# Kernel optimization log

Hardware: AMD Instinct MI355X
Metric: run time of the kernel (lower is better)

## Reference

```python
import jax, jax.numpy as jnp
import numpy as np

# ---- static config (matches torch module defaults) ----
SPATIAL = np.array([[100, 100], [50, 50], [25, 25], [13, 13]], dtype=np.int64)  # [L,2] (H,W)
EMBED, HEADS, LEVELS, POINTS = 256, 8, 4, 4
HEAD_DIM = EMBED // HEADS
TOTAL_POINTS = HEADS * LEVELS * POINTS
BS, LQ = 32, 300
LV = int((SPATIAL[:, 0] * SPATIAL[:, 1]).sum())  # 13294


def setup_inputs() -> dict:
    key = jax.random.key(0)
    ks = jax.random.split(key, 12)
    s = 1.0 / np.sqrt(EMBED)
    return {
        "query": jax.random.normal(ks[0], (BS, LQ, EMBED), jnp.float32),
        "reference_points": jax.random.uniform(ks[1], (BS, LQ, LEVELS, 2), jnp.float32),
        "value": jax.random.normal(ks[2], (BS, LV, EMBED), jnp.float32),
        "value_spatial_shapes": jnp.asarray(SPATIAL),
        # learned parameters (torch: Linear weight [out,in] -> stored here as [in,out])
        "W_off": jax.random.normal(ks[3], (EMBED, TOTAL_POINTS * 2), jnp.float32) * 0.01,
        "b_off": jax.random.normal(ks[4], (TOTAL_POINTS * 2,), jnp.float32) * 0.01,
        "W_attn": jax.random.normal(ks[5], (EMBED, TOTAL_POINTS), jnp.float32) * s,
        "b_attn": jnp.zeros((TOTAL_POINTS,), jnp.float32),
        "W_val": jax.random.normal(ks[6], (EMBED, EMBED), jnp.float32) * s,
        "b_val": jnp.zeros((EMBED,), jnp.float32),
        "W_out": jax.random.normal(ks[7], (EMBED, EMBED), jnp.float32) * s,
        "b_out": jnp.zeros((EMBED,), jnp.float32),
    }


def _bilinear_sample(v, grid, H, W):
    """F.grid_sample(mode='bilinear', padding_mode='zeros', align_corners=False).
    v: [H*W, c], grid: [Lq, P, 2] in [-1, 1] (x, y). Returns [Lq, P, c]."""
    x = (grid[..., 0] + 1.0) * 0.5 * W - 0.5
    y = (grid[..., 1] + 1.0) * 0.5 * H - 0.5
    x0f, y0f = jnp.floor(x), jnp.floor(y)
    lx, ly = x - x0f, y - y0f
    x0, y0 = x0f.astype(jnp.int32), y0f.astype(jnp.int32)

    def gather(iy, ix):
        valid = ((iy >= 0) & (iy < H) & (ix >= 0) & (ix < W)).astype(v.dtype)[..., None]
        idx = jnp.clip(iy, 0, H - 1) * W + jnp.clip(ix, 0, W - 1)
        return v[idx] * valid

    return (gather(y0, x0) * ((1 - ly) * (1 - lx))[..., None]
            + gather(y0, x0 + 1) * ((1 - ly) * lx)[..., None]
            + gather(y0 + 1, x0) * (ly * (1 - lx))[..., None]
            + gather(y0 + 1, x0 + 1) * (ly * lx)[..., None])


def _ms_deform_attn_core(value, sampling_grids, attention_weights):
    """value: [bs, Lv, H, c]; sampling_grids: [bs, Lq, H, L, P, 2] in [-1,1];
    attention_weights: [bs, Lq, H, L, P] -> output [bs, Lq, H*c]."""
    bs, Lq = sampling_grids.shape[:2]
    samples = []
    start = 0
    for lvl in range(LEVELS):
        H, W = int(SPATIAL[lvl, 0]), int(SPATIAL[lvl, 1])
        # [bs, HW, nh, c] -> [bs*nh, HW, c]
        v_l = value[:, start:start + H * W]
        v_l = v_l.transpose(0, 2, 1, 3).reshape(bs * HEADS, H * W, HEAD_DIM)
        # [bs, Lq, nh, P, 2] -> [bs*nh, Lq, P, 2]
        g_l = sampling_grids[:, :, :, lvl].transpose(0, 2, 1, 3, 4).reshape(bs * HEADS, Lq, POINTS, 2)
        samples.append(jax.vmap(lambda vv, gg: _bilinear_sample(vv, gg, H, W))(v_l, g_l))
        start += H * W
    stacked = jnp.stack(samples, axis=2)  # [bs*nh, Lq, L, P, c]
    aw = attention_weights.transpose(0, 2, 1, 3, 4).reshape(bs * HEADS, Lq, LEVELS, POINTS)
    out = (stacked * aw[..., None]).sum(axis=(2, 3))  # [bs*nh, Lq, c]
    return out.reshape(bs, HEADS, Lq, HEAD_DIM).transpose(0, 2, 1, 3).reshape(bs, Lq, EMBED)


def reference(query, reference_points, value, value_spatial_shapes,
              W_off, b_off, W_attn, b_attn, W_val, b_val, W_out, b_out):
    bs, Lq = query.shape[:2]
    Lv = value.shape[1]

    value_p = (value @ W_val + b_val).reshape(bs, Lv, HEADS, HEAD_DIM)

    offsets = (query @ W_off + b_off).reshape(bs, Lq, HEADS, LEVELS, POINTS, 2)
    attn = jax.nn.softmax((query @ W_attn + b_attn).reshape(bs, Lq, HEADS, LEVELS * POINTS), axis=-1)
    attn = attn.reshape(bs, Lq, HEADS, LEVELS, POINTS)

    # offset_normalizer = flip(spatial_shapes) -> (W, H) per level
    norm = jnp.asarray(SPATIAL[:, ::-1].copy(), jnp.float32)  # [L, 2]
    sampling_locations = (reference_points[:, :, None, :, None, :]
                          + offsets / norm[None, None, None, :, None, :])
    sampling_grids = 2.0 * sampling_locations - 1.0

    out = _ms_deform_attn_core(value_p, sampling_grids, attn)
    return out @ W_out + b_out
```

## Files before the change

kernel.cpp:

```cpp
#include <hip/hip_runtime.h>
#include <hip/hip_bf16.h>

#define BS_   32
#define LQ_   300
#define LV_   13294
#define EMBED_ 256
#define HEADS_ 8
#define HEAD_DIM_ 32
#define NCHUNK_ 13294
#define PSTRIDE_ 512

typedef __attribute__((ext_vector_type(8))) short bf16x8;
typedef __attribute__((ext_vector_type(4))) float f32x4;

__device__ inline short f2bf(float f) {
  union { float f; unsigned u; } x; x.f = f;
  return (short)((x.u + 0x7FFF + ((x.u >> 16) & 1)) >> 16);
}
__device__ inline short f2bf_i(float f) {
  union { __hip_bfloat16 h; short s; } u;
  u.h = __float2bfloat16(f);
  return u.s;
}
__device__ inline float bf2f(short s) {
  union { unsigned u; float f; } x; x.u = ((unsigned)(unsigned short)s) << 16;
  return x.f;
}

__device__ __forceinline__ void gld_lds16(const void* g, void* l) {
  __builtin_amdgcn_global_load_lds(
      (const __attribute__((address_space(1))) unsigned int*)g,
      (__attribute__((address_space(3))) unsigned int*)l, 16, 0, 0);
}

__global__ void convert_wt(const float* __restrict__ W, short* __restrict__ Wt,
                           int Nsrc) {
  const int n = blockIdx.x;
  const int k = threadIdx.x;
  Wt[n * 256 + k] = (n < Nsrc) ? f2bf(W[k * Nsrc + n]) : (short)0;
}

__global__ __launch_bounds__(512, 2) void gemm_value_persist(
    const float* __restrict__ A, const short* __restrict__ Wt,
    const float* __restrict__ bias, short* __restrict__ Vp) {
  __shared__ float As[2][32 * 256];

  const int tid = threadIdx.x;
  const int lane = tid & 63;
  const int w = tid >> 6;
  const int lr = lane & 15;
  const int lkq = lane >> 4;

  bf16x8 bfr[2][8];
#pragma unroll
  for (int nf = 0; nf < 2; ++nf) {
    const size_t bbase = (size_t)(w * 32 + nf * 16 + lr) * 256 + lkq * 8;
#pragma unroll
    for (int kt = 0; kt < 8; ++kt)
      bfr[nf][kt] = *(const bf16x8*)(Wt + bbase + kt * 32);
  }
  float bv[2];
#pragma unroll
  for (int nf = 0; nf < 2; ++nf) bv[nf] = bias[w * 32 + nf * 16 + lr];

  auto stage = [&](int buf, int c) {
    const float* src = A + (size_t)c * (32 * 256);
#pragma unroll
    for (int i = 0; i < 4; ++i) {
      const int r = w * 4 + i;
      gld_lds16(src + r * 256 + ((lane ^ (r & 7)) * 4), &As[buf][r * 256]);
    }
  };

  const int c0 = blockIdx.x;
  stage(0, c0);
  asm volatile("s_waitcnt vmcnt(0)" ::: "memory");
  __syncthreads();

  int cb = 0;
  for (int c = c0; c < NCHUNK_; c += PSTRIDE_) {
    const int nxt = c + PSTRIDE_;
    if (nxt < NCHUNK_) stage(cb ^ 1, nxt);

    f32x4 acc[2][2];
#pragma unroll
    for (int i = 0; i < 2; ++i)
#pragma unroll
      for (int jj = 0; jj < 2; ++jj) acc[i][jj] = (f32x4){0.f, 0.f, 0.f, 0.f};

    const float* as = &As[cb][0];
#pragma unroll
    for (int kt = 0; kt < 8; ++kt) {
      const int r0 = lr;
      const int r1 = 16 + lr;
      const int g = kt * 8 + lkq * 2;
      const f32x4 a00 = *(const f32x4*)(as + r0 * 256 + (((g    ) ^ (r0 & 7)) * 4));
      const f32x4 a01 = *(const f32x4*)(as + r0 * 256 + (((g + 1) ^ (r0 & 7)) * 4));
      const f32x4 a10 = *(const f32x4*)(as + r1 * 256 + (((g    ) ^ (r1 & 7)) * 4));
      const f32x4 a11 = *(const f32x4*)(as + r1 * 256 + (((g + 1) ^ (r1 & 7)) * 4));
      bf16x8 af0, af1;
#pragma unroll
      for (int i = 0; i < 4; ++i) {
        af0[i]     = f2bf_i(a00[i]);
        af0[i + 4] = f2bf_i(a01[i]);
        af1[i]     = f2bf_i(a10[i]);
        af1[i + 4] = f2bf_i(a11[i]);
      }
      acc[0][0] = __builtin_amdgcn_mfma_f32_16x16x32_bf16(af0, bfr[0][kt], acc[0][0], 0, 0, 0);
      acc[0][1] = __builtin_amdgcn_mfma_f32_16x16x32_bf16(af0, bfr[1][kt], acc[0][1], 0, 0, 0);
      acc[1][0] = __builtin_amdgcn_mfma_f32_16x16x32_bf16(af1, bfr[0][kt], acc[1][0], 0, 0, 0);
      acc[1][1] = __builtin_amdgcn_mfma_f32_16x16x32_bf16(af1, bfr[1][kt], acc[1][1], 0, 0, 0);
    }

#pragma unroll
    for (int mf = 0; mf < 2; ++mf)
#pragma unroll
      for (int rr = 0; rr < 4; ++rr) {
        const unsigned m = (unsigned)c * 32 + mf * 16 + lkq * 4 + rr;
        const unsigned b_ = m / LV_;
        const unsigned pos = m - b_ * LV_;
        const size_t rowbase = ((size_t)(b_ * HEADS_ + w) * LV_ + pos) * HEAD_DIM_;
#pragma unroll
        for (int nf = 0; nf < 2; ++nf)
          Vp[rowbase + nf * 16 + lr] = f2bf(acc[mf][nf][rr] + bv[nf]);
      }

    if (nxt < NCHUNK_) {
      asm volatile("s_waitcnt vmcnt(16)" ::: "memory");
      asm volatile("s_barrier" ::: "memory");
    }
    cb ^= 1;
  }
}

__global__ __launch_bounds__(256, 2) void gemm_qproj(
    const float* __restrict__ A, const short* __restrict__ Wt,
    const float* __restrict__ bias, float* __restrict__ C,
    int ldc, int Nbias) {
  __shared__ float As[64 * 256];

  const int tid = threadIdx.x;
  const int lane = tid & 63;
  const int w = tid >> 6;
  const int n0 = w * 64;
  const size_t m0 = (size_t)blockIdx.x * 64;
  const int lr = lane & 15;
  const int lkq = lane >> 4;

#pragma unroll
  for (int i = 0; i < 16; ++i) {
    const int row = w * 16 + i;
    gld_lds16(A + (m0 + row) * 256 + ((lane ^ (row & 7)) * 4), As + row * 256);
  }

  bf16x8 bfr[4][8];
#pragma unroll
  for (int nf = 0; nf < 4; ++nf) {
    const size_t bbase = (size_t)(n0 + nf * 16 + lr) * 256 + lkq * 8;
#pragma unroll
    for (int kt = 0; kt < 8; ++kt)
      bfr[nf][kt] = *(const bf16x8*)(Wt + bbase + kt * 32);
  }

  f32x4 acc[4][4];
#pragma unroll
  for (int i = 0; i < 4; ++i)
#pragma unroll
    for (int jj = 0; jj < 4; ++jj) acc[i][jj] = (f32x4){0.f, 0.f, 0.f, 0.f};

  __syncthreads();

#pragma unroll
  for (int kt = 0; kt < 8; ++kt) {
#pragma unroll
    for (int mf = 0; mf < 4; ++mf) {
      const int row = mf * 16 + lr;
      const int gbase = kt * 8 + lkq * 2;
      const f32x4 a0 = *(const f32x4*)(As + row * 256 + ((gbase) ^ (row & 7)) * 4);
      const f32x4 a1 = *(const f32x4*)(As + row * 256 + ((gbase + 1) ^ (row & 7)) * 4);
      bf16x8 af;
#pragma unroll
      for (int i = 0; i < 4; ++i) {
        af[i]     = f2bf_i(a0[i]);
        af[i + 4] = f2bf_i(a1[i]);
      }
#pragma unroll
      for (int nf = 0; nf < 4; ++nf)
        acc[mf][nf] = __builtin_amdgcn_mfma_f32_16x16x32_bf16(af, bfr[nf][kt], acc[mf][nf], 0, 0, 0);
    }
  }

  float bv[4];
#pragma unroll
  for (int nf = 0; nf < 4; ++nf) {
    const int n = n0 + nf * 16 + lr;
    bv[nf] = (n < Nbias) ? bias[n] : 0.f;
  }
  const int lq4 = lkq * 4;
#pragma unroll
  for (int mf = 0; mf < 4; ++mf)
#pragma unroll
    for (int r = 0; r < 4; ++r) {
      const size_t m = m0 + mf * 16 + lq4 + r;
#pragma unroll
      for (int nf = 0; nf < 4; ++nf) {
        const int n = n0 + nf * 16 + lr;
        C[m * ldc + n] = acc[mf][nf][r] + bv[nf];
      }
    }
}

__global__ void softmax16(const float* __restrict__ logits,
                          float* __restrict__ attn, int ngroups) {
  const int g = blockIdx.x * blockDim.x + threadIdx.x;
  if (g >= ngroups) return;
  const int row = g >> 3, h = g & 7;
  const float* in = logits + (size_t)row * 256 + h * 16;
  float v[16];
  float m = -1e30f;
#pragma unroll
  for (int i = 0; i < 16; ++i) { v[i] = in[i]; m = fmaxf(m, v[i]); }
  float s = 0.f;
#pragma unroll
  for (int i = 0; i < 16; ++i) { v[i] = __expf(v[i] - m); s += v[i]; }
  const float inv = 1.0f / s;
  float* out = attn + (size_t)g * 16;
#pragma unroll
  for (int i = 0; i < 16; ++i) out[i] = v[i] * inv;
}

__global__ __launch_bounds__(256) void msda_sample(
    const float* __restrict__ ref_pts,
    const float* __restrict__ offsets,
    const float* __restrict__ attn,
    const short* __restrict__ value_p,
    float* __restrict__ tmp)
{
  const int t = blockIdx.x * 256 + threadIdx.x;
  const int c8 = t & 3;
  const int h = (t >> 2) & 7;
  const int row = t >> 5;
  const int b = row / LQ_;

  const int HS[4] = {100, 50, 25, 13};
  const int START[4] = {0, 10000, 12500, 13125};

  const float* offr = offsets + (size_t)row * 256 + h * 32;
  const float* attr = attn + (size_t)row * 128 + h * 16;
  const float* refr = ref_pts + (size_t)row * 8;

  float acc[8];
#pragma unroll
  for (int jj = 0; jj < 8; ++jj) acc[jj] = 0.f;

#pragma unroll
  for (int l = 0; l < 4; ++l) {
    const int HH = HS[l];
    const int WW = HS[l];
    const float fH = (float)HH, fW = (float)WW;
    const float rx = refr[l * 2 + 0];
    const float ry = refr[l * 2 + 1];
    const short* vbase =
        value_p + ((size_t)(b * HEADS_ + h) * LV_ + START[l]) * HEAD_DIM_ + c8 * 8;
#pragma unroll
    for (int p = 0; p < 4; ++p) {
      const float ox = offr[(l * 4 + p) * 2 + 0];
      const float oy = offr[(l * 4 + p) * 2 + 1];
      const float x = (rx + ox / fW) * fW - 0.5f;
      const float y = (ry + oy / fH) * fH - 0.5f;
      const float x0f = floorf(x), y0f = floorf(y);
      const float fx = x - x0f, fy = y - y0f;
      const int x0 = (int)x0f, y0 = (int)y0f;
      const float wgt = attr[l * 4 + p];
      const float iy0 = (y0 >= 0 && y0 < HH) ? 1.f : 0.f;
      const float iy1 = (y0 + 1 >= 0 && y0 + 1 < HH) ? 1.f : 0.f;
      const float ix0 = (x0 >= 0 && x0 < WW) ? 1.f : 0.f;
      const float ix1 = (x0 + 1 >= 0 && x0 + 1 < WW) ? 1.f : 0.f;
      const float w00 = (1.f - fy) * (1.f - fx) * wgt * iy0 * ix0;
      const float w01 = (1.f - fy) * fx * wgt * iy0 * ix1;
      const float w10 = fy * (1.f - fx) * wgt * iy1 * ix0;
      const float w11 = fy * fx * wgt * iy1 * ix1;
      const int xc0 = min(max(x0, 0), WW - 1);
      const int xc1 = min(max(x0 + 1, 0), WW - 1);
      const int yc0 = min(max(y0, 0), HH - 1);
      const int yc1 = min(max(y0 + 1, 0), HH - 1);
      const bf16x8 q00 = *(const bf16x8*)(vbase + (size_t)(yc0 * WW + xc0) * HEAD_DIM_);
      const bf16x8 q01 = *(const bf16x8*)(vbase + (size_t)(yc0 * WW + xc1) * HEAD_DIM_);
      const bf16x8 q10 = *(const bf16x8*)(vbase + (size_t)(yc1 * WW + xc0) * HEAD_DIM_);
      const bf16x8 q11 = *(const bf16x8*)(vbase + (size_t)(yc1 * WW + xc1) * HEAD_DIM_);
#pragma unroll
      for (int jj = 0; jj < 8; ++jj) {
        acc[jj] += w00 * bf2f(q00[jj]) + w01 * bf2f(q01[jj]) +
                   w10 * bf2f(q10[jj]) + w11 * bf2f(q11[jj]);
      }
    }
  }
  float* o = tmp + (size_t)row * 256 + h * 32 + c8 * 8;
  f32x4 o0 = {acc[0], acc[1], acc[2], acc[3]};
  f32x4 o1 = {acc[4], acc[5], acc[6], acc[7]};
  *(f32x4*)(o) = o0;
  *(f32x4*)(o + 4) = o1;
}

extern "C" void kernel_launch(void* const* d_in, const int* in_sizes, int n_in,
                              void* d_out, int out_size, void* d_ws, size_t ws_size,
                              hipStream_t stream) {
  const float* query  = (const float*)d_in[0];
  const float* refpts = (const float*)d_in[1];
  const float* value  = (const float*)d_in[2];
  const float* W_off  = (const float*)d_in[4];
  const float* b_off  = (const float*)d_in[5];
  const float* W_attn = (const float*)d_in[6];
  const float* b_attn = (const float*)d_in[7];
  const float* W_val  = (const float*)d_in[8];
  const float* b_val  = (const float*)d_in[9];
  const float* W_out  = (const float*)d_in[10];
  const float* b_out  = (const float*)d_in[11];
  float* out = (float*)d_out;

  char* ws = (char*)d_ws;
  short* value_p = (short*)ws;
  size_t off = (size_t)BS_ * HEADS_ * LV_ * HEAD_DIM_ * 2;
  float* offsets = (float*)(ws + off); off += (size_t)BS_ * LQ_ * 256 * 4;
  float* attn    = (float*)(ws + off); off += (size_t)BS_ * LQ_ * 128 * 4;
  float* tmp     = (float*)(ws + off); off += (size_t)BS_ * LQ_ * 256 * 4;

  short* WtA = (short*)value_p;
  short* WtB = (short*)value_p + 256 * 256;
  float* logits = tmp;
  short* WtV = (short*)tmp;
  short* WtO = (short*)value_p;

  const int MQ = BS_ * LQ_;

  convert_wt<<<256, 256, 0, stream>>>(W_off, WtA, 256);
  convert_wt<<<256, 256, 0, stream>>>(W_attn, WtB, 128);
  gemm_qproj<<<MQ / 64, 256, 0, stream>>>(query, WtA, b_off, offsets, 256, 256);
  gemm_qproj<<<MQ / 64, 256, 0, stream>>>(query, WtB, b_attn, logits, 256, 128);
  softmax16<<<(MQ * HEADS_ + 255) / 256, 256, 0, stream>>>(logits, attn, MQ * HEADS_);
  convert_wt<<<256, 256, 0, stream>>>(W_val, WtV, 256);
  gemm_value_persist<<<PSTRIDE_, 512, 0, stream>>>(value, WtV, b_val, value_p);
  msda_sample<<<(MQ * 32) / 256, 256, 0, stream>>>(refpts, offsets, attn, value_p, tmp);
  convert_wt<<<256, 256, 0, stream>>>(W_out, WtO, 256);
  gemm_qproj<<<MQ / 64, 256, 0, stream>>>(tmp, WtO, b_out, out, 256, 256);
}
```

Baseline: 228.1 us.

## Fuse offset/attn projections into one GEMM and fold softmax into sampler

```diff
diff --git a/kernel.cpp b/kernel.cpp
--- a/kernel.cpp
+++ b/kernel.cpp
@@ -38,6 +38,15 @@
   const int n = blockIdx.x;
   const int k = threadIdx.x;
   Wt[n * 256 + k] = (n < Nsrc) ? f2bf(W[k * Nsrc + n]) : (short)0;
+}
+
+__global__ void convert_wq(const float* __restrict__ W_off,
+                           const float* __restrict__ W_attn,
+                           short* __restrict__ Wt) {
+  const int n = blockIdx.x;
+  const int k = threadIdx.x;
+  Wt[n * 256 + k] = (n < 256) ? f2bf(W_off[k * 256 + n])
+                              : f2bf(W_attn[k * 128 + (n - 256)]);
 }
 
 __global__ __launch_bounds__(512, 2) void gemm_value_persist(
@@ -133,10 +142,10 @@
   }
 }
 
-__global__ __launch_bounds__(256, 2) void gemm_qproj(
+__global__ __launch_bounds__(384, 2) void gemm_qproj2(
     const float* __restrict__ A, const short* __restrict__ Wt,
-    const float* __restrict__ bias, float* __restrict__ C,
-    int ldc, int Nbias) {
+    const float* __restrict__ b_off, const float* __restrict__ b_attn,
+    float* __restrict__ offs, float* __restrict__ logits) {
   __shared__ float As[64 * 256];
 
   const int tid = threadIdx.x;
@@ -147,10 +156,12 @@
   const int lr = lane & 15;
   const int lkq = lane >> 4;
 
-#pragma unroll
-  for (int i = 0; i < 16; ++i) {
-    const int row = w * 16 + i;
-    gld_lds16(A + (m0 + row) * 256 + ((lane ^ (row & 7)) * 4), As + row * 256);
+  if (w < 4) {
+#pragma unroll
+    for (int i = 0; i < 16; ++i) {
+      const int row = w * 16 + i;
+      gld_lds16(A + (m0 + row) * 256 + ((lane ^ (row & 7)) * 4), As + row * 256);
+    }
   }
 
   bf16x8 bfr[4][8];
@@ -194,7 +205,7 @@
 #pragma unroll
   for (int nf = 0; nf < 4; ++nf) {
     const int n = n0 + nf * 16 + lr;
-    bv[nf] = (n < Nbias) ? bias[n] : 0.f;
+    bv[nf] = (n < 256) ? b_off[n] : b_attn[n - 256];
   }
   const int lq4 = lkq * 4;
 #pragma unroll
@@ -205,53 +216,123 @@
 #pragma unroll
       for (int nf = 0; nf < 4; ++nf) {
         const int n = n0 + nf * 16 + lr;
-        C[m * ldc + n] = acc[mf][nf][r] + bv[nf];
-      }
-    }
-}
-
-__global__ void softmax16(const float* __restrict__ logits,
-                          float* __restrict__ attn, int ngroups) {
-  const int g = blockIdx.x * blockDim.x + threadIdx.x;
-  if (g >= ngroups) return;
-  const int row = g >> 3, h = g & 7;
-  const float* in = logits + (size_t)row * 256 + h * 16;
-  float v[16];
-  float m = -1e30f;
-#pragma unroll
-  for (int i = 0; i < 16; ++i) { v[i] = in[i]; m = fmaxf(m, v[i]); }
-  float s = 0.f;
-#pragma unroll
-  for (int i = 0; i < 16; ++i) { v[i] = __expf(v[i] - m); s += v[i]; }
-  const float inv = 1.0f / s;
-  float* out = attn + (size_t)g * 16;
-#pragma unroll
-  for (int i = 0; i < 16; ++i) out[i] = v[i] * inv;
-}
-
-__global__ __launch_bounds__(256) void msda_sample(
+        if (n < 256) offs[m * 256 + n] = acc[mf][nf][r] + bv[nf];
+        else         logits[m * 128 + (n - 256)] = acc[mf][nf][r] + bv[nf];
+      }
+    }
+}
+
+__global__ __launch_bounds__(256, 2) void gemm_qproj(
+    const float* __restrict__ A, const short* __restrict__ Wt,
+    const float* __restrict__ bias, float* __restrict__ C) {
+  __shared__ float As[64 * 256];
+
+  const int tid = threadIdx.x;
+  const int lane = tid & 63;
+  const int w = tid >> 6;
+  const int n0 = w * 64;
+  const size_t m0 = (size_t)blockIdx.x * 64;
+  const int lr = lane & 15;
+  const int lkq = lane >> 4;
+
+#pragma unroll
+  for (int i = 0; i < 16; ++i) {
+    const int row = w * 16 + i;
+    gld_lds16(A + (m0 + row) * 256 + ((lane ^ (row & 7)) * 4), As + row * 256);
+  }
+
+  bf16x8 bfr[4][8];
+#pragma unroll
+  for (int nf = 0; nf < 4; ++nf) {
+    const size_t bbase = (size_t)(n0 + nf * 16 + lr) * 256 + lkq * 8;
+#pragma unroll
+    for (int kt = 0; kt < 8; ++kt)
+      bfr[nf][kt] = *(const bf16x8*)(Wt + bbase + kt * 32);
+  }
+
+  f32x4 acc[4][4];
+#pragma unroll
+  for (int i = 0; i < 4; ++i)
+#pragma unroll
+    for (int jj = 0; jj < 4; ++jj) acc[i][jj] = (f32x4){0.f, 0.f, 0.f, 0.f};
+
+  __syncthreads();
+
+#pragma unroll
+  for (int kt = 0; kt < 8; ++kt) {
+#pragma unroll
+    for (int mf = 0; mf < 4; ++mf) {
+      const int row = mf * 16 + lr;
+      const int gbase = kt * 8 + lkq * 2;
+      const f32x4 a0 = *(const f32x4*)(As + row * 256 + ((gbase) ^ (row & 7)) * 4);
+      const f32x4 a1 = *(const f32x4*)(As + row * 256 + ((gbase + 1) ^ (row & 7)) * 4);
+      bf16x8 af;
+#pragma unroll
+      for (int i = 0; i < 4; ++i) {
+        af[i]     = f2bf_i(a0[i]);
+        af[i + 4] = f2bf_i(a1[i]);
+      }
+#pragma unroll
+      for (int nf = 0; nf < 4; ++nf)
+        acc[mf][nf] = __builtin_amdgcn_mfma_f32_16x16x32_bf16(af, bfr[nf][kt], acc[mf][nf], 0, 0, 0);
+    }
+  }
+
+  float bv[4];
+#pragma unroll
+  for (int nf = 0; nf < 4; ++nf) bv[nf] = bias[n0 + nf * 16 + lr];
+  const int lq4 = lkq * 4;
+#pragma unroll
+  for (int mf = 0; mf < 4; ++mf)
+#pragma unroll
+    for (int r = 0; r < 4; ++r) {
+      const size_t m = m0 + mf * 16 + lq4 + r;
+#pragma unroll
+      for (int nf = 0; nf < 4; ++nf) {
+        const int n = n0 + nf * 16 + lr;
+        C[m * 256 + n] = acc[mf][nf][r] + bv[nf];
+      }
+    }
+}
+
+__global__ __launch_bounds__(256) void msda_sample_fused(
     const float* __restrict__ ref_pts,
     const float* __restrict__ offsets,
-    const float* __restrict__ attn,
+    const float* __restrict__ logits,
     const short* __restrict__ value_p,
     float* __restrict__ tmp)
 {
   const int t = blockIdx.x * 256 + threadIdx.x;
-  const int c8 = t & 3;
-  const int h = (t >> 2) & 7;
-  const int row = t >> 5;
+  const int c16 = t & 1;
+  const int h = (t >> 1) & 7;
+  const int row = t >> 4;
   const int b = row / LQ_;
 
   const int HS[4] = {100, 50, 25, 13};
   const int START[4] = {0, 10000, 12500, 13125};
 
+  const float* lg = logits + (size_t)row * 128 + h * 16;
+  float wv[16];
+  float mx = -1e30f;
+#pragma unroll
+  for (int i = 0; i < 4; ++i) {
+    const f32x4 v = *(const f32x4*)(lg + i * 4);
+#pragma unroll
+    for (int jj = 0; jj < 4; ++jj) { wv[i * 4 + jj] = v[jj]; mx = fmaxf(mx, v[jj]); }
+  }
+  float sum = 0.f;
+#pragma unroll
+  for (int i = 0; i < 16; ++i) { wv[i] = __expf(wv[i] - mx); sum += wv[i]; }
+  const float inv = 1.0f / sum;
+#pragma unroll
+  for (int i = 0; i < 16; ++i) wv[i] *= inv;
+
   const float* offr = offsets + (size_t)row * 256 + h * 32;
-  const float* attr = attn + (size_t)row * 128 + h * 16;
   const float* refr = ref_pts + (size_t)row * 8;
 
-  float acc[8];
-#pragma unroll
-  for (int jj = 0; jj < 8; ++jj) acc[jj] = 0.f;
+  float acc[16];
+#pragma unroll
+  for (int jj = 0; jj < 16; ++jj) acc[jj] = 0.f;
 
 #pragma unroll
   for (int l = 0; l < 4; ++l) {
@@ -261,7 +342,7 @@
     const float rx = refr[l * 2 + 0];
     const float ry = refr[l * 2 + 1];
     const short* vbase =
-        value_p + ((size_t)(b * HEADS_ + h) * LV_ + START[l]) * HEAD_DIM_ + c8 * 8;
+        value_p + ((size_t)(b * HEADS_ + h) * LV_ + START[l]) * HEAD_DIM_ + c16 * 16;
 #pragma unroll
     for (int p = 0; p < 4; ++p) {
       const float ox = offr[(l * 4 + p) * 2 + 0];
@@ -271,7 +352,7 @@
       const float x0f = floorf(x), y0f = floorf(y);
       const float fx = x - x0f, fy = y - y0f;
       const int x0 = (int)x0f, y0 = (int)y0f;
-      const float wgt = attr[l * 4 + p];
+      const float wgt = wv[l * 4 + p];
       const float iy0 = (y0 >= 0 && y0 < HH) ? 1.f : 0.f;
       const float iy1 = (y0 + 1 >= 0 && y0 + 1 < HH) ? 1.f : 0.f;
       const float ix0 = (x0 >= 0 && x0 < WW) ? 1.f : 0.f;
@@ -284,22 +365,33 @@
       const int xc1 = min(max(x0 + 1, 0), WW - 1);
       const int yc0 = min(max(y0, 0), HH - 1);
       const int yc1 = min(max(y0 + 1, 0), HH - 1);
-      const bf16x8 q00 = *(const bf16x8*)(vbase + (size_t)(yc0 * WW + xc0) * HEAD_DIM_);
-      const bf16x8 q01 = *(const bf16x8*)(vbase + (size_t)(yc0 * WW + xc1) * HEAD_DIM_);
-      const bf16x8 q10 = *(const bf16x8*)(vbase + (size_t)(yc1 * WW + xc0) * HEAD_DIM_);
-      const bf16x8 q11 = *(const bf16x8*)(vbase + (size_t)(yc1 * WW + xc1) * HEAD_DIM_);
+      const short* p00 = vbase + (size_t)(yc0 * WW + xc0) * HEAD_DIM_;
+      const short* p01 = vbase + (size_t)(yc0 * WW + xc1) * HEAD_DIM_;
+      const short* p10 = vbase + (size_t)(yc1 * WW + xc0) * HEAD_DIM_;
+      const short* p11 = vbase + (size_t)(yc1 * WW + xc1) * HEAD_DIM_;
+      const bf16x8 q00a = *(const bf16x8*)(p00);
+      const bf16x8 q00b = *(const bf16x8*)(p00 + 8);
+      const bf16x8 q01a = *(const bf16x8*)(p01);
+      const bf16x8 q01b = *(const bf16x8*)(p01 + 8);
+      const bf16x8 q10a = *(const bf16x8*)(p10);
+      const bf16x8 q10b = *(const bf16x8*)(p10 + 8);
+      const bf16x8 q11a = *(const bf16x8*)(p11);
+      const bf16x8 q11b = *(const bf16x8*)(p11 + 8);
 #pragma unroll
       for (int jj = 0; jj < 8; ++jj) {
-        acc[jj] += w00 * bf2f(q00[jj]) + w01 * bf2f(q01[jj]) +
-                   w10 * bf2f(q10[jj]) + w11 * bf2f(q11[jj]);
-      }
-    }
-  }
-  float* o = tmp + (size_t)row * 256 + h * 32 + c8 * 8;
-  f32x4 o0 = {acc[0], acc[1], acc[2], acc[3]};
-  f32x4 o1 = {acc[4], acc[5], acc[6], acc[7]};
-  *(f32x4*)(o) = o0;
-  *(f32x4*)(o + 4) = o1;
+        acc[jj] += w00 * bf2f(q00a[jj]) + w01 * bf2f(q01a[jj]) +
+                   w10 * bf2f(q10a[jj]) + w11 * bf2f(q11a[jj]);
+        acc[jj + 8] += w00 * bf2f(q00b[jj]) + w01 * bf2f(q01b[jj]) +
+                       w10 * bf2f(q10b[jj]) + w11 * bf2f(q11b[jj]);
+      }
+    }
+  }
+  float* o = tmp + (size_t)row * 256 + h * 32 + c16 * 16;
+#pragma unroll
+  for (int i = 0; i < 4; ++i) {
+    f32x4 v = {acc[i * 4], acc[i * 4 + 1], acc[i * 4 + 2], acc[i * 4 + 3]};
+    *(f32x4*)(o + i * 4) = v;
+  }
 }
 
 extern "C" void kernel_launch(void* const* d_in, const int* in_sizes, int n_in,
@@ -322,25 +414,20 @@
   short* value_p = (short*)ws;
   size_t off = (size_t)BS_ * HEADS_ * LV_ * HEAD_DIM_ * 2;
   float* offsets = (float*)(ws + off); off += (size_t)BS_ * LQ_ * 256 * 4;
-  float* attn    = (float*)(ws + off); off += (size_t)BS_ * LQ_ * 128 * 4;
+  float* logits  = (float*)(ws + off); off += (size_t)BS_ * LQ_ * 128 * 4;
   float* tmp     = (float*)(ws + off); off += (size_t)BS_ * LQ_ * 256 * 4;
 
-  short* WtA = (short*)value_p;
-  short* WtB = (short*)value_p + 256 * 256;
-  float* logits = tmp;
+  short* WtQ = (short*)value_p;
   short* WtV = (short*)tmp;
   short* WtO = (short*)value_p;
 
   const int MQ = BS_ * LQ_;
 
-  convert_wt<<<256, 256, 0, stream>>>(W_off, WtA, 256);
-  convert_wt<<<256, 256, 0, stream>>>(W_attn, WtB, 128);
-  gemm_qproj<<<MQ / 64, 256, 0, stream>>>(query, WtA, b_off, offsets, 256, 256);
-  gemm_qproj<<<MQ / 64, 256, 0, stream>>>(query, WtB, b_attn, logits, 256, 128);
-  softmax16<<<(MQ * HEADS_ + 255) / 256, 256, 0, stream>>>(logits, attn, MQ * HEADS_);
+  convert_wq<<<384, 256, 0, stream>>>(W_off, W_attn, WtQ);
+  gemm_qproj2<<<MQ / 64, 384, 0, stream>>>(query, WtQ, b_off, b_attn, offsets, logits);
   convert_wt<<<256, 256, 0, stream>>>(W_val, WtV, 256);
   gemm_value_persist<<<PSTRIDE_, 512, 0, stream>>>(value, WtV, b_val, value_p);
-  msda_sample<<<(MQ * 32) / 256, 256, 0, stream>>>(refpts, offsets, attn, value_p, tmp);
+  msda_sample_fused<<<(MQ * 16) / 256, 256, 0, stream>>>(refpts, offsets, logits, value_p, tmp);
   convert_wt<<<256, 256, 0, stream>>>(W_out, WtO, 256);
-  gemm_qproj<<<MQ / 64, 256, 0, stream>>>(tmp, WtO, b_out, out, 256, 256);
-}
+  gemm_qproj<<<MQ / 64, 256, 0, stream>>>(tmp, WtO, b_out, out);
+}
```

New measurement: 242.9 us. +6.5%, slower.
